# Kernel tuning notes

Hardware: AMD Instinct MI355X
Metric: run time of the kernel (lower is better)

The kernel has to match this reference:

```python
import jax, jax.numpy as jnp
import numpy as np

Q, B, S, D, H, DFF = 300, 2, 4096, 256, 8, 2048
HD = D // H
SMOOTH = 8.0


def _ln(x, g, b):
    m = x.mean(-1, keepdims=True)
    v = ((x - m) ** 2).mean(-1, keepdims=True)
    return (x - m) / jnp.sqrt(v + 1e-5) * g + b


def _mha(q, k, v, Wi, bi, Wo, bo, bias=None):
    # q: [L,B,D], k/v: [S,B,D]; torch nn.MultiheadAttention math (eval mode)
    L, Bb, Dd = q.shape
    Sl = k.shape[0]
    Wq, Wk, Wv = jnp.split(Wi, 3, axis=0)
    bq, bk, bv = jnp.split(bi, 3)
    qp = ((q @ Wq.T + bq) * (HD ** -0.5)).reshape(L, Bb * H, HD).transpose(1, 0, 2)
    kp = (k @ Wk.T + bk).reshape(Sl, Bb * H, HD).transpose(1, 0, 2)
    vp = (v @ Wv.T + bv).reshape(Sl, Bb * H, HD).transpose(1, 0, 2)
    logits = jnp.einsum('bld,bsd->bls', qp, kp)  # [B*H, L, S]
    if bias is not None:
        logits = logits + bias  # Gaussian distance bias added pre-softmax
    attn = jax.nn.softmax(logits, axis=-1)
    out = jnp.einsum('bls,bsd->bld', attn, vp).transpose(1, 0, 2).reshape(L, Bb, Dd)
    return out @ Wo.T + bo


def setup_inputs():
    key = jax.random.key(0)
    ks = iter(jax.random.split(key, 48))
    def nrm(shape, s=1.0):
        return jax.random.normal(next(ks), shape, dtype=jnp.float32) * s
    inp = {}
    inp['grid'] = jax.random.uniform(next(ks), (S, 1, 2), dtype=jnp.float32) * 32.0
    inp['h_w'] = jax.random.uniform(next(ks), (B, 2), dtype=jnp.float32) * 800.0
    inp['tgt'] = nrm((Q, B, D))
    inp['memory'] = nrm((S, B, D))
    inp['pos'] = nrm((S, B, D))
    inp['query_pos'] = nrm((Q, B, D))
    inp['reshape_outputs1'] = jax.random.randint(next(ks), (Q, 4), 0, 3, dtype=jnp.int32)
    inp['reshape_outputs2'] = jax.random.randint(next(ks), (Q, 4), 0, 3, dtype=jnp.int32)
    w = 0.02
    inp['sa_Wi'] = nrm((3 * D, D), w); inp['sa_bi'] = jnp.zeros((3 * D,), jnp.float32)
    inp['sa_Wo'] = nrm((D, D), w); inp['sa_bo'] = jnp.zeros((D,), jnp.float32)
    inp['ca_Wi'] = nrm((3 * D, D), w); inp['ca_bi'] = jnp.zeros((3 * D,), jnp.float32)
    inp['ca_Wo'] = nrm((D, D), w); inp['ca_bo'] = jnp.zeros((D,), jnp.float32)
    inp['W1'] = nrm((DFF, D), w); inp['b1'] = jnp.zeros((DFF,), jnp.float32)
    inp['W2'] = nrm((D, DFF), w); inp['b2'] = jnp.zeros((D,), jnp.float32)
    for n in ['n1', 'n2', 'n3', 'n4']:
        inp[n + 'g'] = jnp.ones((D,), jnp.float32)
        inp[n + 'b'] = jnp.zeros((D,), jnp.float32)
    inp['p1_W0'] = nrm((256, 256), w); inp['p1_b0'] = jnp.zeros((256,), jnp.float32)
    inp['p1_W1'] = nrm((256, 256), w); inp['p1_b1'] = jnp.zeros((256,), jnp.float32)
    inp['p1_W2'] = nrm((2, 256), w); inp['p1_b2'] = jnp.zeros((2,), jnp.float32)
    inp['p2W'] = nrm((16, D), w); inp['p2b'] = jnp.zeros((16,), jnp.float32)
    inp['p3W'] = nrm((16, D), w); inp['p3b'] = jnp.zeros((16,), jnp.float32)
    return inp


def reference(grid, h_w, tgt, memory, pos, query_pos, reshape_outputs1, reshape_outputs2,
              sa_Wi, sa_bi, sa_Wo, sa_bo, ca_Wi, ca_bi, ca_Wo, ca_bo,
              W1, b1, W2, b2, n1g, n1b, n2g, n2b, n3g, n3b, n4g, n4b,
              p1_W0, p1_b0, p1_W1, p1_b1, p1_W2, p1_b2, p2W, p2b, p3W, p3b):
    out = _ln(tgt + query_pos, n4g, n4b)                          # [Q,B,D]
    point_offset = out @ p2W.T + p2b                              # [Q,B,16]
    qk = tgt + query_pos
    tgt2 = _mha(qk, qk, tgt, sa_Wi, sa_bi, sa_Wo, sa_bo)
    x = _ln(tgt + tgt2, n1g, n1b)
    # point1 MLP (layer_index == 0)
    h1 = jax.nn.relu(out @ p1_W0.T + p1_b0)
    h2 = jax.nn.relu(h1 @ p1_W1.T + p1_b1)
    ref_inter = h2 @ p1_W2.T + p1_b2                              # [Q,B,2]
    ref = h_w * jax.nn.sigmoid(ref_inter) / 32.0                  # [Q,B,2]
    ref = jnp.tile(ref, (1, 1, 8))                                # [Q,B,16]
    point = (ref + point_offset).reshape(Q, B * 8, 2)             # [Q,B*8,2]
    dist = (point[:, None, :, :] - grid[None]) ** 2               # [Q,S,B*8,2]
    scale = out @ p3W.T + p3b                                     # type3: [Q,B,16]
    scale = (scale * scale).reshape(Q, B * 8, 2)[:, None]         # [Q,1,B*8,2]
    dist = (dist * scale).sum(-1)                                 # [Q,S,B*8]
    gaussian = -jnp.abs(dist) / SMOOTH
    gbias = jnp.transpose(gaussian, (2, 0, 1))                    # [B*8,Q,S]
    # masked object query from reshape_outputs
    oq = jnp.transpose(query_pos, (1, 0, 2))                      # [B,Q,D]
    m1 = jnp.any(reshape_outputs1 == 0, axis=1)                   # [Q]
    m2 = jnp.any(reshape_outputs2 == 0, axis=1)
    oq1 = jnp.where(m1[:, None], 0.0, oq[0])
    oq2 = jnp.where(m2[:, None], 0.0, oq[1])
    new_oq = jnp.stack([oq1, oq2], axis=1)                        # [Q,2,D]
    tgt2 = _mha(x + query_pos, memory + pos, memory, ca_Wi, ca_bi, ca_Wo, ca_bo, bias=gbias)
    tgt3 = _mha(x + new_oq, memory + pos, memory, ca_Wi, ca_bi, ca_Wo, ca_bo, bias=gbias)
    x = _ln(x + tgt2, n2g, n2b)
    ff = jax.nn.relu(x @ W1.T + b1) @ W2.T + b2
    x = _ln(x + ff, n3g, n3b)
    return (x, ref_inter, ref, tgt3)
```

## Files before the change

### kernel.cpp

```cpp
#include <hip/hip_runtime.h>
#include <hip/hip_bf16.h>
#include <math.h>

#define QN 300
#define BN 2
#define SN 4096
#define DN 256
#define HN 8
#define HD 32
#define BH 16
#define DFF 2048

__device__ inline float wred_max(float v) {
#pragma unroll
    for (int m = 32; m > 0; m >>= 1) v = fmaxf(v, __shfl_xor(v, m));
    return v;
}
__device__ inline float wred_sum(float v) {
#pragma unroll
    for (int m = 32; m > 0; m >>= 1) v += __shfl_xor(v, m);
    return v;
}

__global__ __launch_bounds__(256) void addln_kernel(
    const float* __restrict__ a, const float* __restrict__ b,
    const float* __restrict__ g, const float* __restrict__ be,
    float* __restrict__ out_ln, float* __restrict__ out_sum)
{
    int row = blockIdx.x;
    int t = threadIdx.x;
    float v = a[row * DN + t] + b[row * DN + t];
    if (out_sum) out_sum[row * DN + t] = v;
    float s = wred_sum(v);
    float s2 = wred_sum(v * v);
    __shared__ float ws1[4], ws2[4];
    int wave = t >> 6, lane = t & 63;
    if (lane == 0) { ws1[wave] = s; ws2[wave] = s2; }
    __syncthreads();
    float S1 = ws1[0] + ws1[1] + ws1[2] + ws1[3];
    float S2 = ws2[0] + ws2[1] + ws2[2] + ws2[3];
    float mean = S1 * (1.0f / DN);
    float var = S2 * (1.0f / DN) - mean * mean;
    float inv = rsqrtf(var + 1e-5f);
    out_ln[row * DN + t] = (v - mean) * inv * g[t] + be[t];
}

__global__ void addvec_kernel(const float* __restrict__ a, const float* __restrict__ b,
                              float* __restrict__ c, int n4)
{
    int i = blockIdx.x * blockDim.x + threadIdx.x;
    int stride = gridDim.x * blockDim.x;
    for (; i < n4; i += stride) {
        float4 x = ((const float4*)a)[i];
        float4 y = ((const float4*)b)[i];
        float4 z; z.x = x.x + y.x; z.y = x.y + y.y; z.z = x.z + y.z; z.w = x.w + y.w;
        ((float4*)c)[i] = z;
    }
}

__global__ __launch_bounds__(256) void build_xq_xo(
    const float* __restrict__ x1, const float* __restrict__ qp,
    const int* __restrict__ ro1, const int* __restrict__ ro2,
    float* __restrict__ xq, float* __restrict__ xo)
{
    int row = blockIdx.x, t = threadIdx.x;
    int q = row >> 1, b = row & 1;
    const int* ro = b ? ro2 : ro1;
    bool msk = (ro[q * 4 + 0] == 0) || (ro[q * 4 + 1] == 0) ||
               (ro[q * 4 + 2] == 0) || (ro[q * 4 + 3] == 0);
    float xv = x1[row * DN + t], qv = qp[row * DN + t];
    xq[row * DN + t] = xv + qv;
    xo[row * DN + t] = xv + (msk ? 0.0f : qv);
}

template <int MODE>
__global__ __launch_bounds__(256) void gemm_nt(
    const float* __restrict__ A, const float* __restrict__ W,
    const float* __restrict__ bias, float* __restrict__ C,
    int M, int N, int K, int seqLen, float scale)
{
    __shared__ float As[16][68];
    __shared__ float Bs[16][68];
    int bm = blockIdx.x * 64;
    int bn = blockIdx.y * 64;
    int t = threadIdx.x;
    int lr = t >> 2;
    int lc = (t & 3) << 2;
    int tm = (t >> 4) << 2;
    int tn = (t & 15) << 2;
    float acc[4][4] = {};
    for (int k0 = 0; k0 < K; k0 += 16) {
        int arow = bm + lr;
        float4 av = make_float4(0, 0, 0, 0);
        if (arow < M) av = *(const float4*)&A[(size_t)arow * K + k0 + lc];
        float4 bv = *(const float4*)&W[(size_t)(bn + lr) * K + k0 + lc];
        __syncthreads();
        As[lc + 0][lr] = av.x; As[lc + 1][lr] = av.y; As[lc + 2][lr] = av.z; As[lc + 3][lr] = av.w;
        Bs[lc + 0][lr] = bv.x; Bs[lc + 1][lr] = bv.y; Bs[lc + 2][lr] = bv.z; Bs[lc + 3][lr] = bv.w;
        __syncthreads();
#pragma unroll
        for (int kk = 0; kk < 16; kk++) {
            float4 a = *(const float4*)&As[kk][tm];
            float4 b = *(const float4*)&Bs[kk][tn];
            acc[0][0] = fmaf(a.x, b.x, acc[0][0]); acc[0][1] = fmaf(a.x, b.y, acc[0][1]);
            acc[0][2] = fmaf(a.x, b.z, acc[0][2]); acc[0][3] = fmaf(a.x, b.w, acc[0][3]);
            acc[1][0] = fmaf(a.y, b.x, acc[1][0]); acc[1][1] = fmaf(a.y, b.y, acc[1][1]);
            acc[1][2] = fmaf(a.y, b.z, acc[1][2]); acc[1][3] = fmaf(a.y, b.w, acc[1][3]);
            acc[2][0] = fmaf(a.z, b.x, acc[2][0]); acc[2][1] = fmaf(a.z, b.y, acc[2][1]);
            acc[2][2] = fmaf(a.z, b.z, acc[2][2]); acc[2][3] = fmaf(a.z, b.w, acc[2][3]);
            acc[3][0] = fmaf(a.w, b.x, acc[3][0]); acc[3][1] = fmaf(a.w, b.y, acc[3][1]);
            acc[3][2] = fmaf(a.w, b.z, acc[3][2]); acc[3][3] = fmaf(a.w, b.w, acc[3][3]);
        }
    }
#pragma unroll
    for (int i = 0; i < 4; i++) {
        int m = bm + tm + i;
        if (m >= M) continue;
#pragma unroll
        for (int j = 0; j < 4; j++) {
            int n = bn + tn + j;
            float v = acc[i][j] + bias[n];
            if (MODE == 1) v = fmaxf(v, 0.0f);
            if (MODE == 2) {
                v *= scale;
                int b = m & 1, seq = m >> 1, h = n >> 5, hd = n & 31;
                C[((size_t)(b * 8 + h) * seqLen + seq) * 32 + hd] = v;
            } else {
                C[(size_t)m * N + n] = v;
            }
        }
    }
}

template <int MODE>
__global__ __launch_bounds__(256) void gemm_small(
    const float* __restrict__ A, const float* __restrict__ W,
    const float* __restrict__ bias, float* __restrict__ C,
    int M, int N, int K, int seqLen, float scale)
{
    __shared__ float As[16][36];
    __shared__ float Bs[16][36];
    int bm = blockIdx.x * 32;
    int bn = blockIdx.y * 32;
    int t = threadIdx.x;
    int sr = (t & 127) >> 2;
    int sc = (t & 3) << 2;
    bool isB = t >= 128;
    int tm = (t >> 4) << 1;
    int tn = (t & 15) << 1;
    float acc[2][2] = {};
    int srcRow = (isB ? bn : bm) + sr;
    int lim = isB ? N : M;
    const float* src = isB ? W : A;
    for (int k0 = 0; k0 < K; k0 += 16) {
        float4 v = make_float4(0, 0, 0, 0);
        if (srcRow < lim) v = *(const float4*)&src[(size_t)srcRow * K + k0 + sc];
        __syncthreads();
        float (*Ts)[36] = isB ? Bs : As;
        Ts[sc + 0][sr] = v.x; Ts[sc + 1][sr] = v.y; Ts[sc + 2][sr] = v.z; Ts[sc + 3][sr] = v.w;
        __syncthreads();
#pragma unroll
        for (int kk = 0; kk < 16; kk++) {
            float2 a = *(const float2*)&As[kk][tm];
            float2 b = *(const float2*)&Bs[kk][tn];
            acc[0][0] = fmaf(a.x, b.x, acc[0][0]); acc[0][1] = fmaf(a.x, b.y, acc[0][1]);
            acc[1][0] = fmaf(a.y, b.x, acc[1][0]); acc[1][1] = fmaf(a.y, b.y, acc[1][1]);
        }
    }
#pragma unroll
    for (int i = 0; i < 2; i++) {
        int m = bm + tm + i;
        if (m >= M) continue;
#pragma unroll
        for (int j = 0; j < 2; j++) {
            int n = bn + tn + j;
            float v = acc[i][j] + bias[n];
            if (MODE == 1) v = fmaxf(v, 0.0f);
            if (MODE == 2) {
                v *= scale;
                int b = m & 1, seq = m >> 1, h = n >> 5, hd = n & 31;
                C[((size_t)(b * 8 + h) * seqLen + seq) * 32 + hd] = v;
            } else {
                C[(size_t)m * N + n] = v;
            }
        }
    }
}

__global__ __launch_bounds__(64) void small_heads(
    const float* __restrict__ ln4, const float* __restrict__ h2,
    const float* __restrict__ p2W, const float* __restrict__ p2b,
    const float* __restrict__ p3W, const float* __restrict__ p3b,
    const float* __restrict__ p1W2, const float* __restrict__ p1b2,
    const float* __restrict__ h_w,
    float* __restrict__ ref_inter_out, float* __restrict__ ref_out,
    float* __restrict__ point, float* __restrict__ scale2)
{
    int row = blockIdx.x;
    int lane = threadIdx.x;
    __shared__ float rA[DN], rH[DN];
    __shared__ float po[16], sc[16], ri[2];
#pragma unroll
    for (int i = 0; i < 4; i++) {
        rA[lane + i * 64] = ln4[row * DN + lane + i * 64];
        rH[lane + i * 64] = h2[row * DN + lane + i * 64];
    }
    __syncthreads();
    for (int j = 0; j < 16; j++) {
        float p = 0;
#pragma unroll
        for (int i = 0; i < 4; i++) { int d = lane + i * 64; p = fmaf(rA[d], p2W[j * DN + d], p); }
        p = wred_sum(p);
        if (lane == 0) po[j] = p + p2b[j];
    }
    for (int j = 0; j < 16; j++) {
        float p = 0;
#pragma unroll
        for (int i = 0; i < 4; i++) { int d = lane + i * 64; p = fmaf(rA[d], p3W[j * DN + d], p); }
        p = wred_sum(p);
        if (lane == 0) sc[j] = p + p3b[j];
    }
    for (int j = 0; j < 2; j++) {
        float p = 0;
#pragma unroll
        for (int i = 0; i < 4; i++) { int d = lane + i * 64; p = fmaf(rH[d], p1W2[j * DN + d], p); }
        p = wred_sum(p);
        if (lane == 0) ri[j] = p + p1b2[j];
    }
    __syncthreads();
    int q = row >> 1, b = row & 1;
    float sig0 = 1.0f / (1.0f + expf(-ri[0]));
    float sig1 = 1.0f / (1.0f + expf(-ri[1]));
    float rx = h_w[b * 2 + 0] * sig0 * (1.0f / 32.0f);
    float ry = h_w[b * 2 + 1] * sig1 * (1.0f / 32.0f);
    if (lane < 2) ref_inter_out[row * 2 + lane] = ri[lane];
    if (lane < 16) {
        float rc = (lane & 1) ? ry : rx;
        ref_out[row * 16 + lane] = rc;
        int pidx = (q * 16 + b * 8 + (lane >> 1)) * 2 + (lane & 1);
        point[pidx] = rc + po[lane];
        float s = sc[lane];
        scale2[pidx] = s * s;
    }
}

template <bool BIAS>
__global__ __launch_bounds__(256) void attn_split(
    const float* __restrict__ qp, const float* __restrict__ kp, const float* __restrict__ vp,
    const float* __restrict__ point, const float* __restrict__ scale2,
    const float* __restrict__ grid_xy,
    float* __restrict__ pacc, float* __restrict__ pm, float* __restrict__ pl,
    int S, int L, int tilesPerChunk, int ROWS)
{
    const int bh = blockIdx.y;
    const int q0 = blockIdx.x * 16;
    const int chunk = blockIdx.z;
    const int nT = (S + 63) >> 6;
    const int t_begin = chunk * tilesPerChunk;
    const int t_end = min(nT, t_begin + tilesPerChunk);

    __shared__ float Qs[16][36];
    __shared__ float Ks[64][36];
    __shared__ float Vsf[64 * 32];
    __shared__ float Ps[16][68];
    __shared__ float sf_s[16];
    __shared__ float pt_s[16][2], sc_s[16][2];

    int t = threadIdx.x;
    int wave = t >> 6, lane = t & 63;

    {
        int qi = t >> 4, d = (t & 15) * 2;
        int gq = q0 + qi;
        float2 v = make_float2(0, 0);
        if (gq < L) v = *(const float2*)&qp[((size_t)bh * L + gq) * 32 + d];
        Qs[qi][d] = v.x; Qs[qi][d + 1] = v.y;
        if (BIAS && t < 32) {
            int qi2 = t >> 1, c = t & 1;
            int gq2 = q0 + qi2;
            pt_s[qi2][c] = (gq2 < L) ? point[(gq2 * 16 + bh) * 2 + c] : 0.0f;
            sc_s[qi2][c] = (gq2 < L) ? scale2[(gq2 * 16 + bh) * 2 + c] : 0.0f;
        }
    }
    float m_run[4], l_run[4];
#pragma unroll
    for (int r = 0; r < 4; r++) { m_run[r] = -INFINITY; l_run[r] = 0.0f; }
    int pq = t >> 4, pd = t & 15;
    float2 acc = make_float2(0.0f, 0.0f);
    __syncthreads();

    for (int tt = t_begin; tt < t_end; tt++) {
        int s0 = tt << 6;
#pragma unroll
        for (int rep = 0; rep < 2; rep++) {
            int f = t + rep * 256;
            int s = f >> 3, dc = (f & 7) * 4;
            int gs = s0 + s;
            float4 kv = make_float4(0, 0, 0, 0), vv = make_float4(0, 0, 0, 0);
            if (gs < S) {
                kv = *(const float4*)&kp[((size_t)bh * S + gs) * 32 + dc];
                vv = *(const float4*)&vp[((size_t)bh * S + gs) * 32 + dc];
            }
            Ks[s][dc + 0] = kv.x; Ks[s][dc + 1] = kv.y; Ks[s][dc + 2] = kv.z; Ks[s][dc + 3] = kv.w;
            Vsf[s * 32 + dc + 0] = vv.x; Vsf[s * 32 + dc + 1] = vv.y;
            Vsf[s * 32 + dc + 2] = vv.z; Vsf[s * 32 + dc + 3] = vv.w;
        }
        float gx = 0, gy = 0;
        if (BIAS) {
            int gs = s0 + lane;
            if (gs < S) { gx = grid_xy[gs * 2 + 0]; gy = grid_xy[gs * 2 + 1]; }
        }
        __syncthreads();

        float kreg[32];
#pragma unroll
        for (int d4 = 0; d4 < 8; d4++) {
            float4 kk = *(const float4*)&Ks[lane][d4 * 4];
            kreg[d4 * 4 + 0] = kk.x; kreg[d4 * 4 + 1] = kk.y;
            kreg[d4 * 4 + 2] = kk.z; kreg[d4 * 4 + 3] = kk.w;
        }
        bool svalid = (s0 + lane) < S;
#pragma unroll
        for (int r = 0; r < 4; r++) {
            int qi = wave * 4 + r;
            float sum = 0;
#pragma unroll
            for (int d4 = 0; d4 < 8; d4++) {
                float4 qv = *(const float4*)&Qs[qi][d4 * 4];
                sum = fmaf(qv.x, kreg[d4 * 4 + 0], sum);
                sum = fmaf(qv.y, kreg[d4 * 4 + 1], sum);
                sum = fmaf(qv.z, kreg[d4 * 4 + 2], sum);
                sum = fmaf(qv.w, kreg[d4 * 4 + 3], sum);
            }
            if (BIAS) {
                float dx = pt_s[qi][0] - gx, dy = pt_s[qi][1] - gy;
                sum -= (sc_s[qi][0] * dx * dx + sc_s[qi][1] * dy * dy) * 0.125f;
            }
            float l = svalid ? sum : -INFINITY;
            float tmax = wred_max(l);
            float m_new = fmaxf(m_run[r], tmax);
            float p = expf(l - m_new);
            float psum = wred_sum(p);
            float sfv = expf(m_run[r] - m_new);
            l_run[r] = l_run[r] * sfv + psum;
            m_run[r] = m_new;
            Ps[qi][lane] = p;
            if (lane == 0) sf_s[qi] = sfv;
        }
        __syncthreads();

        {
            float sfv = sf_s[pq];
            acc.x *= sfv; acc.y *= sfv;
#pragma unroll
            for (int s4 = 0; s4 < 16; s4++) {
                float4 p4 = *(const float4*)&Ps[pq][s4 * 4];
                float2 v0 = *(const float2*)&Vsf[(s4 * 4 + 0) * 32 + pd * 2];
                float2 v1 = *(const float2*)&Vsf[(s4 * 4 + 1) * 32 + pd * 2];
                float2 v2 = *(const float2*)&Vsf[(s4 * 4 + 2) * 32 + pd * 2];
                float2 v3 = *(const float2*)&Vsf[(s4 * 4 + 3) * 32 + pd * 2];
                acc.x = fmaf(p4.x, v0.x, acc.x); acc.y = fmaf(p4.x, v0.y, acc.y);
                acc.x = fmaf(p4.y, v1.x, acc.x); acc.y = fmaf(p4.y, v1.y, acc.y);
                acc.x = fmaf(p4.z, v2.x, acc.x); acc.y = fmaf(p4.z, v2.y, acc.y);
                acc.x = fmaf(p4.w, v3.x, acc.x); acc.y = fmaf(p4.w, v3.y, acc.y);
            }
        }
        __syncthreads();
    }

    if (lane == 0) {
#pragma unroll
        for (int r = 0; r < 4; r++) {
            int row = q0 + wave * 4 + r;
            int pidx = (chunk * 16 + bh) * ROWS + row;
            pm[pidx] = m_run[r];
            pl[pidx] = l_run[r];
        }
    }
    {
        int row = q0 + pq;
        int pidx = (chunk * 16 + bh) * ROWS + row;
        *(float2*)&pacc[(size_t)pidx * 32 + pd * 2] = acc;
    }
}

__global__ __launch_bounds__(256) void attn_combine(
    const float* __restrict__ pacc, const float* __restrict__ pm, const float* __restrict__ pl,
    float* __restrict__ outbuf, int NS, int ROWS, int L)
{
    int gid = blockIdx.x * 256 + threadIdx.x;
    if (gid >= 16 * L * 32) return;
    int d = gid & 31;
    int pr = gid >> 5;
    int bh = pr / L;
    int row = pr - bh * L;
    float M = -INFINITY;
    for (int c = 0; c < NS; c++) M = fmaxf(M, pm[(c * 16 + bh) * ROWS + row]);
    float Lt = 0.0f, a = 0.0f;
    for (int c = 0; c < NS; c++) {
        int pidx = (c * 16 + bh) * ROWS + row;
        float w = expf(pm[pidx] - M);
        Lt = fmaf(pl[pidx], w, Lt);
        a = fmaf(pacc[(size_t)pidx * 32 + d], w, a);
    }
    int b = bh >> 3, h = bh & 7;
    outbuf[((size_t)row * BN + b) * DN + h * 32 + d] = a / Lt;
}

#define OFF_QK      0
#define OFF_LN4     153600
#define OFF_H1      307200
#define OFF_TMP     307200
#define OFF_H2      460800
#define OFF_POINT   614400
#define OFF_SCALE2  624000
#define OFF_SAQ     633600
#define OFF_SAK     787200
#define OFF_SAV     940800
#define OFF_AOUT    1094400
#define OFF_X1      1248000
#define OFF_MP      1401600
#define OFF_PACC    1401600
#define OFF_PM      2646784
#define OFF_PL      2685696
#define OFF_CAK     3498752
#define OFF_CAV     5595904
#define OFF_XQ      7693056
#define OFF_XO      7846656
#define OFF_AOUT2   8000256
#define OFF_AOUT3   8153856
#define OFF_X2      8307456
#define OFF_FFH     8461056

extern "C" void kernel_launch(void* const* d_in, const int* in_sizes, int n_in,
                              void* d_out, int out_size, void* d_ws, size_t ws_size,
                              hipStream_t stream)
{
    const float* grid_in   = (const float*)d_in[0];
    const float* h_w       = (const float*)d_in[1];
    const float* tgt       = (const float*)d_in[2];
    const float* memory    = (const float*)d_in[3];
    const float* pos       = (const float*)d_in[4];
    const float* query_pos = (const float*)d_in[5];
    const int*   ro1       = (const int*)d_in[6];
    const int*   ro2       = (const int*)d_in[7];
    const float* sa_Wi = (const float*)d_in[8];
    const float* sa_bi = (const float*)d_in[9];
    const float* sa_Wo = (const float*)d_in[10];
    const float* sa_bo = (const float*)d_in[11];
    const float* ca_Wi = (const float*)d_in[12];
    const float* ca_bi = (const float*)d_in[13];
    const float* ca_Wo = (const float*)d_in[14];
    const float* ca_bo = (const float*)d_in[15];
    const float* W1 = (const float*)d_in[16];
    const float* b1 = (const float*)d_in[17];
    const float* W2 = (const float*)d_in[18];
    const float* b2 = (const float*)d_in[19];
    const float* n1g = (const float*)d_in[20];
    const float* n1b = (const float*)d_in[21];
    const float* n2g = (const float*)d_in[22];
    const float* n2b = (const float*)d_in[23];
    const float* n3g = (const float*)d_in[24];
    const float* n3b = (const float*)d_in[25];
    const float* n4g = (const float*)d_in[26];
    const float* n4b = (const float*)d_in[27];
    const float* p1_W0 = (const float*)d_in[28];
    const float* p1_b0 = (const float*)d_in[29];
    const float* p1_W1 = (const float*)d_in[30];
    const float* p1_b1 = (const float*)d_in[31];
    const float* p1_W2 = (const float*)d_in[32];
    const float* p1_b2 = (const float*)d_in[33];
    const float* p2W = (const float*)d_in[34];
    const float* p2b = (const float*)d_in[35];
    const float* p3W = (const float*)d_in[36];
    const float* p3b = (const float*)d_in[37];

    float* ws  = (float*)d_ws;
    float* out = (float*)d_out;
    const float qscale = 0.1767766952966369f;

    dim3 g600(600), b256(256);
    dim3 gS(19, 8);
    dim3 gFF1(19, 64);
    dim3 gKV(128, 4);

    addln_kernel<<<g600, b256, 0, stream>>>(tgt, query_pos, n4g, n4b, ws + OFF_LN4, ws + OFF_QK);
    gemm_small<1><<<gS, b256, 0, stream>>>(ws + OFF_LN4, p1_W0, p1_b0, ws + OFF_H1, 600, 256, 256, 0, 1.f);
    gemm_small<1><<<gS, b256, 0, stream>>>(ws + OFF_H1, p1_W1, p1_b1, ws + OFF_H2, 600, 256, 256, 0, 1.f);
    small_heads<<<g600, dim3(64), 0, stream>>>(ws + OFF_LN4, ws + OFF_H2, p2W, p2b, p3W, p3b,
                                               p1_W2, p1_b2, h_w,
                                               out + 153600, out + 154800,
                                               ws + OFF_POINT, ws + OFF_SCALE2);
    gemm_small<2><<<gS, b256, 0, stream>>>(ws + OFF_QK, sa_Wi,          sa_bi,       ws + OFF_SAQ, 600, 256, 256, 300, qscale);
    gemm_small<2><<<gS, b256, 0, stream>>>(ws + OFF_QK, sa_Wi + 65536,  sa_bi + 256, ws + OFF_SAK, 600, 256, 256, 300, 1.f);
    gemm_small<2><<<gS, b256, 0, stream>>>(tgt,         sa_Wi + 131072, sa_bi + 512, ws + OFF_SAV, 600, 256, 256, 300, 1.f);
    attn_split<false><<<dim3(19, 16, 2), b256, 0, stream>>>(
        ws + OFF_SAQ, ws + OFF_SAK, ws + OFF_SAV, nullptr, nullptr, nullptr,
        ws + OFF_PACC, ws + OFF_PM, ws + OFF_PL, 300, 300, 3, 304);
    attn_combine<<<g600, b256, 0, stream>>>(ws + OFF_PACC, ws + OFF_PM, ws + OFF_PL,
                                            ws + OFF_AOUT, 2, 304, 300);
    gemm_small<0><<<gS, b256, 0, stream>>>(ws + OFF_AOUT, sa_Wo, sa_bo, ws + OFF_TMP, 600, 256, 256, 0, 1.f);
    addln_kernel<<<g600, b256, 0, stream>>>(tgt, ws + OFF_TMP, n1g, n1b, ws + OFF_X1, nullptr);
    addvec_kernel<<<dim3(2048), b256, 0, stream>>>(memory, pos, ws + OFF_MP, (SN * BN * DN) / 4);
    gemm_nt<2><<<gKV, b256, 0, stream>>>(ws + OFF_MP, ca_Wi + 65536,  ca_bi + 256, ws + OFF_CAK, 8192, 256, 256, 4096, 1.f);
    gemm_nt<2><<<gKV, b256, 0, stream>>>(memory,      ca_Wi + 131072, ca_bi + 512, ws + OFF_CAV, 8192, 256, 256, 4096, 1.f);
    build_xq_xo<<<g600, b256, 0, stream>>>(ws + OFF_X1, query_pos, ro1, ro2, ws + OFF_XQ, ws + OFF_XO);
    gemm_small<2><<<gS, b256, 0, stream>>>(ws + OFF_XQ, ca_Wi, ca_bi, ws + OFF_SAQ, 600, 256, 256, 300, qscale);
    gemm_small<2><<<gS, b256, 0, stream>>>(ws + OFF_XO, ca_Wi, ca_bi, ws + OFF_SAK, 600, 256, 256, 300, qscale);
    attn_split<true><<<dim3(19, 16, 8), b256, 0, stream>>>(
        ws + OFF_SAQ, ws + OFF_CAK, ws + OFF_CAV,
        ws + OFF_POINT, ws + OFF_SCALE2, grid_in,
        ws + OFF_PACC, ws + OFF_PM, ws + OFF_PL, 4096, 300, 8, 304);
    attn_combine<<<g600, b256, 0, stream>>>(ws + OFF_PACC, ws + OFF_PM, ws + OFF_PL,
                                            ws + OFF_AOUT2, 8, 304, 300);
    attn_split<true><<<dim3(19, 16, 8), b256, 0, stream>>>(
        ws + OFF_SAK, ws + OFF_CAK, ws + OFF_CAV,
        ws + OFF_POINT, ws + OFF_SCALE2, grid_in,
        ws + OFF_PACC, ws + OFF_PM, ws + OFF_PL, 4096, 300, 8, 304);
    attn_combine<<<g600, b256, 0, stream>>>(ws + OFF_PACC, ws + OFF_PM, ws + OFF_PL,
                                            ws + OFF_AOUT3, 8, 304, 300);
    gemm_small<0><<<gS, b256, 0, stream>>>(ws + OFF_AOUT2, ca_Wo, ca_bo, ws + OFF_TMP, 600, 256, 256, 0, 1.f);
    gemm_small<0><<<gS, b256, 0, stream>>>(ws + OFF_AOUT3, ca_Wo, ca_bo, out + 164400, 600, 256, 256, 0, 1.f);
    addln_kernel<<<g600, b256, 0, stream>>>(ws + OFF_X1, ws + OFF_TMP, n2g, n2b, ws + OFF_X2, nullptr);
    gemm_small<1><<<gFF1, b256, 0, stream>>>(ws + OFF_X2, W1, b1, ws + OFF_FFH, 600, 2048, 256, 0, 1.f);
    gemm_small<0><<<gS, b256, 0, stream>>>(ws + OFF_FFH, W2, b2, ws + OFF_TMP, 600, 256, 2048, 0, 1.f);
    addln_kernel<<<g600, b256, 0, stream>>>(ws + OFF_X2, ws + OFF_TMP, n3g, n3b, out, nullptr);
}
```

Measured before the change: 711.7 us.

## Use bf16 MFMA for cross-attention K/V projections and one attention pass

Converts memory, memory+pos and the K/V weights to bf16 and computes the cross-attention K/V projections with a 16x16x32 bf16 MFMA GEMM that writes bf16 head-major outputs. The first cross-attention pass reads the bf16 K/V and widens it into shared memory, using a transposed V layout. The second pass is replaced by a new kernel that computes QK^T with MFMA over 64-query tiles, adds the Gaussian bias and runs online softmax. This is meant to cut the FP32 FMA work and the K/V memory traffic, at the cost of bf16 precision in K, V and one set of queries, plus extra conversion kernels.

```diff
diff --git a/kernel.cpp b/kernel.cpp
--- a/kernel.cpp
+++ b/kernel.cpp
@@ -11,15 +11,23 @@
 #define BH 16
 #define DFF 2048
 
-__device__ inline float wred_max(float v) {
-#pragma unroll
-    for (int m = 32; m > 0; m >>= 1) v = fmaxf(v, __shfl_xor(v, m));
-    return v;
-}
+typedef __attribute__((ext_vector_type(8))) short s16x8;
+typedef __attribute__((ext_vector_type(4))) float f32x4;
+
 __device__ inline float wred_sum(float v) {
 #pragma unroll
     for (int m = 32; m > 0; m >>= 1) v += __shfl_xor(v, m);
     return v;
+}
+__device__ inline ushort f2b(float x) {
+    union { __hip_bfloat16 h; ushort u; } c;
+    c.h = __float2bfloat16(x);
+    return c.u;
+}
+__device__ inline float b2f(ushort u) {
+    union { unsigned int i; float f; } c;
+    c.i = ((unsigned int)u) << 16;
+    return c.f;
 }
 
 __global__ __launch_bounds__(256) void addln_kernel(
@@ -45,16 +53,29 @@
     out_ln[row * DN + t] = (v - mean) * inv * g[t] + be[t];
 }
 
-__global__ void addvec_kernel(const float* __restrict__ a, const float* __restrict__ b,
-                              float* __restrict__ c, int n4)
+__global__ void f2bf_kernel(const float* __restrict__ in, ushort* __restrict__ out, int n4)
+{
+    int i = blockIdx.x * blockDim.x + threadIdx.x;
+    int stride = gridDim.x * blockDim.x;
+    for (; i < n4; i += stride) {
+        float4 x = ((const float4*)in)[i];
+        ushort4 o;
+        o.x = f2b(x.x); o.y = f2b(x.y); o.z = f2b(x.z); o.w = f2b(x.w);
+        ((ushort4*)out)[i] = o;
+    }
+}
+__global__ void addvec_bf16_kernel(const float* __restrict__ a, const float* __restrict__ b,
+                                   ushort* __restrict__ out, int n4)
 {
     int i = blockIdx.x * blockDim.x + threadIdx.x;
     int stride = gridDim.x * blockDim.x;
     for (; i < n4; i += stride) {
         float4 x = ((const float4*)a)[i];
         float4 y = ((const float4*)b)[i];
-        float4 z; z.x = x.x + y.x; z.y = x.y + y.y; z.z = x.z + y.z; z.w = x.w + y.w;
-        ((float4*)c)[i] = z;
+        ushort4 o;
+        o.x = f2b(x.x + y.x); o.y = f2b(x.y + y.y);
+        o.z = f2b(x.z + y.z); o.w = f2b(x.w + y.w);
+        ((ushort4*)out)[i] = o;
     }
 }
 
@@ -71,65 +92,6 @@
     float xv = x1[row * DN + t], qv = qp[row * DN + t];
     xq[row * DN + t] = xv + qv;
     xo[row * DN + t] = xv + (msk ? 0.0f : qv);
-}
-
-template <int MODE>
-__global__ __launch_bounds__(256) void gemm_nt(
-    const float* __restrict__ A, const float* __restrict__ W,
-    const float* __restrict__ bias, float* __restrict__ C,
-    int M, int N, int K, int seqLen, float scale)
-{
-    __shared__ float As[16][68];
-    __shared__ float Bs[16][68];
-    int bm = blockIdx.x * 64;
-    int bn = blockIdx.y * 64;
-    int t = threadIdx.x;
-    int lr = t >> 2;
-    int lc = (t & 3) << 2;
-    int tm = (t >> 4) << 2;
-    int tn = (t & 15) << 2;
-    float acc[4][4] = {};
-    for (int k0 = 0; k0 < K; k0 += 16) {
-        int arow = bm + lr;
-        float4 av = make_float4(0, 0, 0, 0);
-        if (arow < M) av = *(const float4*)&A[(size_t)arow * K + k0 + lc];
-        float4 bv = *(const float4*)&W[(size_t)(bn + lr) * K + k0 + lc];
-        __syncthreads();
-        As[lc + 0][lr] = av.x; As[lc + 1][lr] = av.y; As[lc + 2][lr] = av.z; As[lc + 3][lr] = av.w;
-        Bs[lc + 0][lr] = bv.x; Bs[lc + 1][lr] = bv.y; Bs[lc + 2][lr] = bv.z; Bs[lc + 3][lr] = bv.w;
-        __syncthreads();
-#pragma unroll
-        for (int kk = 0; kk < 16; kk++) {
-            float4 a = *(const float4*)&As[kk][tm];
-            float4 b = *(const float4*)&Bs[kk][tn];
-            acc[0][0] = fmaf(a.x, b.x, acc[0][0]); acc[0][1] = fmaf(a.x, b.y, acc[0][1]);
-            acc[0][2] = fmaf(a.x, b.z, acc[0][2]); acc[0][3] = fmaf(a.x, b.w, acc[0][3]);
-            acc[1][0] = fmaf(a.y, b.x, acc[1][0]); acc[1][1] = fmaf(a.y, b.y, acc[1][1]);
-            acc[1][2] = fmaf(a.y, b.z, acc[1][2]); acc[1][3] = fmaf(a.y, b.w, acc[1][3]);
-            acc[2][0] = fmaf(a.z, b.x, acc[2][0]); acc[2][1] = fmaf(a.z, b.y, acc[2][1]);
-            acc[2][2] = fmaf(a.z, b.z, acc[2][2]); acc[2][3] = fmaf(a.z, b.w, acc[2][3]);
-            acc[3][0] = fmaf(a.w, b.x, acc[3][0]); acc[3][1] = fmaf(a.w, b.y, acc[3][1]);
-            acc[3][2] = fmaf(a.w, b.z, acc[3][2]); acc[3][3] = fmaf(a.w, b.w, acc[3][3]);
-        }
-    }
-#pragma unroll
-    for (int i = 0; i < 4; i++) {
-        int m = bm + tm + i;
-        if (m >= M) continue;
-#pragma unroll
-        for (int j = 0; j < 4; j++) {
-            int n = bn + tn + j;
-            float v = acc[i][j] + bias[n];
-            if (MODE == 1) v = fmaxf(v, 0.0f);
-            if (MODE == 2) {
-                v *= scale;
-                int b = m & 1, seq = m >> 1, h = n >> 5, hd = n & 31;
-                C[((size_t)(b * 8 + h) * seqLen + seq) * 32 + hd] = v;
-            } else {
-                C[(size_t)m * N + n] = v;
-            }
-        }
-    }
 }
 
 template <int MODE>
@@ -180,9 +142,58 @@
                 v *= scale;
                 int b = m & 1, seq = m >> 1, h = n >> 5, hd = n & 31;
                 C[((size_t)(b * 8 + h) * seqLen + seq) * 32 + hd] = v;
+            } else if (MODE == 4) {
+                v *= scale;
+                int b = m & 1, seq = m >> 1, h = n >> 5, hd = n & 31;
+                ushort* Cb = (ushort*)C;
+                Cb[((size_t)(b * 8 + h) * seqLen + seq) * 32 + hd] = f2b(v);
             } else {
                 C[(size_t)m * N + n] = v;
             }
+        }
+    }
+}
+
+__global__ __launch_bounds__(256) void gemm_bf16_mfma(
+    const ushort* __restrict__ A, const ushort* __restrict__ W,
+    const float* __restrict__ bias, ushort* __restrict__ C, int seqLen)
+{
+    __shared__ ushort As[64][40];
+    __shared__ ushort Ws[64][40];
+    int bm = blockIdx.x * 64;
+    int bn = blockIdx.y * 64;
+    int t = threadIdx.x;
+    int w = t >> 6, lane = t & 63;
+    int lr = lane & 15, lg = lane >> 4;
+    int sr = t >> 2, sg = t & 3;
+
+    f32x4 acc[4];
+#pragma unroll
+    for (int f = 0; f < 4; f++) acc[f] = (f32x4)0.0f;
+
+    for (int k0 = 0; k0 < 256; k0 += 32) {
+        int4 av = *(const int4*)&A[((size_t)(bm + sr)) * 256 + k0 + sg * 8];
+        int4 wv = *(const int4*)&W[((size_t)(bn + sr)) * 256 + k0 + sg * 8];
+        __syncthreads();
+        *(int4*)&As[sr][sg * 8] = av;
+        *(int4*)&Ws[sr][sg * 8] = wv;
+        __syncthreads();
+        s16x8 af = *(const s16x8*)&As[w * 16 + lr][lg * 8];
+#pragma unroll
+        for (int f = 0; f < 4; f++) {
+            s16x8 bf = *(const s16x8*)&Ws[f * 16 + lr][lg * 8];
+            acc[f] = __builtin_amdgcn_mfma_f32_16x16x32_bf16(af, bf, acc[f], 0, 0, 0);
+        }
+    }
+#pragma unroll
+    for (int f = 0; f < 4; f++) {
+#pragma unroll
+        for (int j = 0; j < 4; j++) {
+            int m = bm + w * 16 + lg * 4 + j;
+            int n = bn + f * 16 + lr;
+            float v = acc[f][j] + bias[n];
+            int b = m & 1, seq = m >> 1, h = n >> 5, hd = n & 31;
+            C[(((size_t)(b * 8 + h) * seqLen) + seq) * 32 + hd] = f2b(v);
         }
     }
 }
@@ -244,9 +255,9 @@
     }
 }
 
-template <bool BIAS>
+template <bool BIAS, bool BF16KV>
 __global__ __launch_bounds__(256) void attn_split(
-    const float* __restrict__ qp, const float* __restrict__ kp, const float* __restrict__ vp,
+    const float* __restrict__ qp, const void* __restrict__ kp_, const void* __restrict__ vp_,
     const float* __restrict__ point, const float* __restrict__ scale2,
     const float* __restrict__ grid_xy,
     float* __restrict__ pacc, float* __restrict__ pm, float* __restrict__ pl,
@@ -261,7 +272,7 @@
 
     __shared__ float Qs[16][36];
     __shared__ float Ks[64][36];
-    __shared__ float Vsf[64 * 32];
+    __shared__ float Vt[32][68];
     __shared__ float Ps[16][68];
     __shared__ float sf_s[16];
     __shared__ float pt_s[16][2], sc_s[16][2];
@@ -291,19 +302,39 @@
 
     for (int tt = t_begin; tt < t_end; tt++) {
         int s0 = tt << 6;
-#pragma unroll
-        for (int rep = 0; rep < 2; rep++) {
-            int f = t + rep * 256;
-            int s = f >> 3, dc = (f & 7) * 4;
+        if (BF16KV) {
+            const ushort* kp = (const ushort*)kp_;
+            const ushort* vp = (const ushort*)vp_;
+            int s = t >> 2, dg = (t & 3) * 8;
             int gs = s0 + s;
-            float4 kv = make_float4(0, 0, 0, 0), vv = make_float4(0, 0, 0, 0);
+            int4 kv = make_int4(0, 0, 0, 0), vv = make_int4(0, 0, 0, 0);
             if (gs < S) {
-                kv = *(const float4*)&kp[((size_t)bh * S + gs) * 32 + dc];
-                vv = *(const float4*)&vp[((size_t)bh * S + gs) * 32 + dc];
-            }
-            Ks[s][dc + 0] = kv.x; Ks[s][dc + 1] = kv.y; Ks[s][dc + 2] = kv.z; Ks[s][dc + 3] = kv.w;
-            Vsf[s * 32 + dc + 0] = vv.x; Vsf[s * 32 + dc + 1] = vv.y;
-            Vsf[s * 32 + dc + 2] = vv.z; Vsf[s * 32 + dc + 3] = vv.w;
+                kv = *(const int4*)&kp[((size_t)bh * S + gs) * 32 + dg];
+                vv = *(const int4*)&vp[((size_t)bh * S + gs) * 32 + dg];
+            }
+            union { int4 v; ushort u[8]; } ck, cv;
+            ck.v = kv; cv.v = vv;
+#pragma unroll
+            for (int jj = 0; jj < 8; jj++) {
+                Ks[s][dg + jj] = b2f(ck.u[jj]);
+                Vt[dg + jj][s] = b2f(cv.u[jj]);
+            }
+        } else {
+            const float* kp = (const float*)kp_;
+            const float* vp = (const float*)vp_;
+#pragma unroll
+            for (int rep = 0; rep < 2; rep++) {
+                int f = t + rep * 256;
+                int s = f >> 3, dc = (f & 7) * 4;
+                int gs = s0 + s;
+                float4 kv = make_float4(0, 0, 0, 0), vv = make_float4(0, 0, 0, 0);
+                if (gs < S) {
+                    kv = *(const float4*)&kp[((size_t)bh * S + gs) * 32 + dc];
+                    vv = *(const float4*)&vp[((size_t)bh * S + gs) * 32 + dc];
+                }
+                Ks[s][dc + 0] = kv.x; Ks[s][dc + 1] = kv.y; Ks[s][dc + 2] = kv.z; Ks[s][dc + 3] = kv.w;
+                Vt[dc + 0][s] = vv.x; Vt[dc + 1][s] = vv.y; Vt[dc + 2][s] = vv.z; Vt[dc + 3][s] = vv.w;
+            }
         }
         float gx = 0, gy = 0;
         if (BIAS) {
@@ -337,11 +368,13 @@
                 sum -= (sc_s[qi][0] * dx * dx + sc_s[qi][1] * dy * dy) * 0.125f;
             }
             float l = svalid ? sum : -INFINITY;
-            float tmax = wred_max(l);
+            float tmax = l;
+#pragma unroll
+            for (int m = 32; m > 0; m >>= 1) tmax = fmaxf(tmax, __shfl_xor(tmax, m));
             float m_new = fmaxf(m_run[r], tmax);
-            float p = expf(l - m_new);
+            float p = __expf(l - m_new);
             float psum = wred_sum(p);
-            float sfv = expf(m_run[r] - m_new);
+            float sfv = __expf(m_run[r] - m_new);
             l_run[r] = l_run[r] * sfv + psum;
             m_run[r] = m_new;
             Ps[qi][lane] = p;
@@ -351,19 +384,19 @@
 
         {
             float sfv = sf_s[pq];
-            acc.x *= sfv; acc.y *= sfv;
+            float ax = acc.x * sfv, ay = acc.y * sfv;
+            int d0 = pd * 2;
 #pragma unroll
             for (int s4 = 0; s4 < 16; s4++) {
                 float4 p4 = *(const float4*)&Ps[pq][s4 * 4];
-                float2 v0 = *(const float2*)&Vsf[(s4 * 4 + 0) * 32 + pd * 2];
-                float2 v1 = *(const float2*)&Vsf[(s4 * 4 + 1) * 32 + pd * 2];
-                float2 v2 = *(const float2*)&Vsf[(s4 * 4 + 2) * 32 + pd * 2];
-                float2 v3 = *(const float2*)&Vsf[(s4 * 4 + 3) * 32 + pd * 2];
-                acc.x = fmaf(p4.x, v0.x, acc.x); acc.y = fmaf(p4.x, v0.y, acc.y);
-                acc.x = fmaf(p4.y, v1.x, acc.x); acc.y = fmaf(p4.y, v1.y, acc.y);
-                acc.x = fmaf(p4.z, v2.x, acc.x); acc.y = fmaf(p4.z, v2.y, acc.y);
-                acc.x = fmaf(p4.w, v3.x, acc.x); acc.y = fmaf(p4.w, v3.y, acc.y);
-            }
+                float4 va = *(const float4*)&Vt[d0][s4 * 4];
+                float4 vb = *(const float4*)&Vt[d0 + 1][s4 * 4];
+                ax = fmaf(p4.x, va.x, ax); ax = fmaf(p4.y, va.y, ax);
+                ax = fmaf(p4.z, va.z, ax); ax = fmaf(p4.w, va.w, ax);
+                ay = fmaf(p4.x, vb.x, ay); ay = fmaf(p4.y, vb.y, ay);
+                ay = fmaf(p4.z, vb.z, ay); ay = fmaf(p4.w, vb.w, ay);
+            }
+            acc.x = ax; acc.y = ay;
         }
         __syncthreads();
     }
@@ -372,15 +405,206 @@
 #pragma unroll
         for (int r = 0; r < 4; r++) {
             int row = q0 + wave * 4 + r;
-            int pidx = (chunk * 16 + bh) * ROWS + row;
+            size_t pidx = (size_t)(chunk * 16 + bh) * ROWS + row;
             pm[pidx] = m_run[r];
             pl[pidx] = l_run[r];
         }
     }
     {
         int row = q0 + pq;
-        int pidx = (chunk * 16 + bh) * ROWS + row;
-        *(float2*)&pacc[(size_t)pidx * 32 + pd * 2] = acc;
+        size_t pidx = (size_t)(chunk * 16 + bh) * ROWS + row;
+        *(float2*)&pacc[pidx * 32 + pd * 2] = acc;
+    }
+}
+
+template <bool BIAS>
+__global__ __launch_bounds__(256) void attn_qkmfma(
+    const ushort* __restrict__ qp, const ushort* __restrict__ kp, const ushort* __restrict__ vp,
+    const float* __restrict__ point, const float* __restrict__ scale2,
+    const float* __restrict__ grid_xy,
+    float* __restrict__ pacc, float* __restrict__ pm, float* __restrict__ pl,
+    int S, int L, int tilesPerChunk, int ROWS)
+{
+    const int bh = blockIdx.y;
+    const int q0 = blockIdx.x * 64;
+    const int chunk = blockIdx.z;
+    const int nT = (S + 63) >> 6;
+    const int t_begin = chunk * tilesPerChunk;
+    const int t_end = min(nT, t_begin + tilesPerChunk);
+
+    __shared__ ushort Ks[64][40];
+    __shared__ float Vt[32][68];
+    __shared__ float Ps[64][68];
+    __shared__ float sf_s[64];
+    __shared__ float gq2[64][2];
+    __shared__ float qc[64][4];
+
+    int t = threadIdx.x;
+    int w = t >> 6, lane = t & 63;
+    int lr = lane & 15, lg = lane >> 4;
+    int sr = t >> 2, sg = t & 3;
+
+    s16x8 qfrag;
+    {
+        int qrow = q0 + w * 16 + lr;
+        if (qrow < L) qfrag = *(const s16x8*)&qp[((size_t)bh * L + qrow) * 32 + lg * 8];
+        else qfrag = (s16x8)(short)0;
+    }
+
+    float px[4], py[4], sx[4], sy[4];
+    if (BIAS) {
+        if (t < 64) {
+            int q = q0 + t;
+            float a = 0, b = 0, c = 0, d = 0;
+            if (q < L) {
+                a = point[(q * 16 + bh) * 2 + 0];
+                b = point[(q * 16 + bh) * 2 + 1];
+                c = scale2[(q * 16 + bh) * 2 + 0];
+                d = scale2[(q * 16 + bh) * 2 + 1];
+            }
+            qc[t][0] = a; qc[t][1] = b; qc[t][2] = c; qc[t][3] = d;
+        }
+        __syncthreads();
+#pragma unroll
+        for (int j = 0; j < 4; j++) {
+            int ql = w * 16 + lg * 4 + j;
+            px[j] = qc[ql][0]; py[j] = qc[ql][1];
+            sx[j] = qc[ql][2]; sy[j] = qc[ql][3];
+        }
+    }
+
+    float m_run[4], l_run[4];
+#pragma unroll
+    for (int j = 0; j < 4; j++) { m_run[j] = -INFINITY; l_run[j] = 0.0f; }
+
+    int q2 = (t >> 3) * 2;
+    int dq = (t & 7) * 4;
+    float accv0[4] = {0, 0, 0, 0};
+    float accv1[4] = {0, 0, 0, 0};
+
+    for (int tt = t_begin; tt < t_end; tt++) {
+        int s0 = tt << 6;
+        int gs = s0 + sr;
+        int4 kv = make_int4(0, 0, 0, 0), vv = make_int4(0, 0, 0, 0);
+        if (gs < S) {
+            kv = *(const int4*)&kp[((size_t)bh * S + gs) * 32 + sg * 8];
+            vv = *(const int4*)&vp[((size_t)bh * S + gs) * 32 + sg * 8];
+        }
+        __syncthreads();
+        *(int4*)&Ks[sr][sg * 8] = kv;
+        {
+            union { int4 v; ushort u[8]; } cv; cv.v = vv;
+            int d0 = sg * 8;
+#pragma unroll
+            for (int jj = 0; jj < 8; jj++) Vt[d0 + jj][sr] = b2f(cv.u[jj]);
+        }
+        if (BIAS && t < 64) {
+            gq2[t][0] = grid_xy[(size_t)(s0 + t) * 2 + 0];
+            gq2[t][1] = grid_xy[(size_t)(s0 + t) * 2 + 1];
+        }
+        __syncthreads();
+
+        f32x4 sfrag[4];
+#pragma unroll
+        for (int f = 0; f < 4; f++) {
+            s16x8 kf = *(const s16x8*)&Ks[f * 16 + lr][lg * 8];
+            sfrag[f] = __builtin_amdgcn_mfma_f32_16x16x32_bf16(qfrag, kf, (f32x4)0.0f, 0, 0, 0);
+        }
+#pragma unroll
+        for (int f = 0; f < 4; f++) {
+            int gsc = s0 + f * 16 + lr;
+            if (BIAS) {
+                float gx = gq2[f * 16 + lr][0];
+                float gy = gq2[f * 16 + lr][1];
+#pragma unroll
+                for (int j = 0; j < 4; j++) {
+                    float dx = px[j] - gx, dy = py[j] - gy;
+                    sfrag[f][j] -= (sx[j] * dx * dx + sy[j] * dy * dy) * 0.125f;
+                }
+            }
+            if (gsc >= S) {
+#pragma unroll
+                for (int j = 0; j < 4; j++) sfrag[f][j] = -INFINITY;
+            }
+        }
+        float sfv[4];
+#pragma unroll
+        for (int j = 0; j < 4; j++) {
+            float mx = fmaxf(fmaxf(sfrag[0][j], sfrag[1][j]), fmaxf(sfrag[2][j], sfrag[3][j]));
+            mx = fmaxf(mx, __shfl_xor(mx, 1));
+            mx = fmaxf(mx, __shfl_xor(mx, 2));
+            mx = fmaxf(mx, __shfl_xor(mx, 4));
+            mx = fmaxf(mx, __shfl_xor(mx, 8));
+            float mnew = fmaxf(m_run[j], mx);
+            sfv[j] = __expf(m_run[j] - mnew);
+            m_run[j] = mnew;
+            float ps = 0.0f;
+#pragma unroll
+            for (int f = 0; f < 4; f++) {
+                float p = __expf(sfrag[f][j] - mnew);
+                sfrag[f][j] = p;
+                ps += p;
+            }
+            ps += __shfl_xor(ps, 1);
+            ps += __shfl_xor(ps, 2);
+            ps += __shfl_xor(ps, 4);
+            ps += __shfl_xor(ps, 8);
+            l_run[j] = l_run[j] * sfv[j] + ps;
+        }
+#pragma unroll
+        for (int f = 0; f < 4; f++) {
+#pragma unroll
+            for (int j = 0; j < 4; j++) {
+                Ps[w * 16 + lg * 4 + j][f * 16 + lr] = sfrag[f][j];
+            }
+        }
+        if (lr == 0) {
+#pragma unroll
+            for (int j = 0; j < 4; j++) sf_s[w * 16 + lg * 4 + j] = sfv[j];
+        }
+        __syncthreads();
+
+        {
+            float sf0 = sf_s[q2], sf1 = sf_s[q2 + 1];
+#pragma unroll
+            for (int d = 0; d < 4; d++) { accv0[d] *= sf0; accv1[d] *= sf1; }
+#pragma unroll
+            for (int s4 = 0; s4 < 16; s4++) {
+                float4 p0 = *(const float4*)&Ps[q2][s4 * 4];
+                float4 p1 = *(const float4*)&Ps[q2 + 1][s4 * 4];
+#pragma unroll
+                for (int d = 0; d < 4; d++) {
+                    float4 v4 = *(const float4*)&Vt[dq + d][s4 * 4];
+                    accv0[d] = fmaf(p0.x, v4.x, accv0[d]);
+                    accv0[d] = fmaf(p0.y, v4.y, accv0[d]);
+                    accv0[d] = fmaf(p0.z, v4.z, accv0[d]);
+                    accv0[d] = fmaf(p0.w, v4.w, accv0[d]);
+                    accv1[d] = fmaf(p1.x, v4.x, accv1[d]);
+                    accv1[d] = fmaf(p1.y, v4.y, accv1[d]);
+                    accv1[d] = fmaf(p1.z, v4.z, accv1[d]);
+                    accv1[d] = fmaf(p1.w, v4.w, accv1[d]);
+                }
+            }
+        }
+    }
+
+    if (lr == 0) {
+#pragma unroll
+        for (int j = 0; j < 4; j++) {
+            int row = q0 + w * 16 + lg * 4 + j;
+            size_t pidx = (size_t)(chunk * 16 + bh) * ROWS + row;
+            pm[pidx] = m_run[j];
+            pl[pidx] = l_run[j];
+        }
+    }
+    {
+        size_t pidx0 = (size_t)(chunk * 16 + bh) * ROWS + (q0 + q2);
+        size_t pidx1 = pidx0 + 1;
+#pragma unroll
+        for (int d = 0; d < 4; d++) {
+            pacc[pidx0 * 32 + dq + d] = accv0[d];
+            pacc[pidx1 * 32 + dq + d] = accv1[d];
+        }
     }
 }
 
@@ -395,13 +619,13 @@
     int bh = pr / L;
     int row = pr - bh * L;
     float M = -INFINITY;
-    for (int c = 0; c < NS; c++) M = fmaxf(M, pm[(c * 16 + bh) * ROWS + row]);
+    for (int c = 0; c < NS; c++) M = fmaxf(M, pm[(size_t)(c * 16 + bh) * ROWS + row]);
     float Lt = 0.0f, a = 0.0f;
     for (int c = 0; c < NS; c++) {
-        int pidx = (c * 16 + bh) * ROWS + row;
-        float w = expf(pm[pidx] - M);
-        Lt = fmaf(pl[pidx], w, Lt);
-        a = fmaf(pacc[(size_t)pidx * 32 + d], w, a);
+        size_t pidx = (size_t)(c * 16 + bh) * ROWS + row;
+        float wgt = __expf(pm[pidx] - M);
+        Lt = fmaf(pl[pidx], wgt, Lt);
+        a = fmaf(pacc[pidx * 32 + d], wgt, a);
     }
     int b = bh >> 3, h = bh & 7;
     outbuf[((size_t)row * BN + b) * DN + h * 32 + d] = a / Lt;
@@ -409,28 +633,32 @@
 
 #define OFF_QK      0
 #define OFF_LN4     153600
-#define OFF_H1      307200
 #define OFF_TMP     307200
-#define OFF_H2      460800
-#define OFF_POINT   614400
-#define OFF_SCALE2  624000
-#define OFF_SAQ     633600
-#define OFF_SAK     787200
-#define OFF_SAV     940800
-#define OFF_AOUT    1094400
-#define OFF_X1      1248000
-#define OFF_MP      1401600
-#define OFF_PACC    1401600
-#define OFF_PM      2646784
-#define OFF_PL      2685696
-#define OFF_CAK     3498752
-#define OFF_CAV     5595904
-#define OFF_XQ      7693056
-#define OFF_XO      7846656
-#define OFF_AOUT2   8000256
-#define OFF_AOUT3   8153856
-#define OFF_X2      8307456
-#define OFF_FFH     8461056
+#define OFF_H1      460800
+#define OFF_H2      614400
+#define OFF_POINT   768000
+#define OFF_SCALE2  777600
+#define OFF_SAQ     787200
+#define OFF_SAK     940800
+#define OFF_SAV     1094400
+#define OFF_AOUT    1248000
+#define OFF_X1      1401600
+#define OFF_PACC    1555200
+#define OFF_PM      2865920
+#define OFF_PL      2906880
+#define OFF_MEMB    2947840
+#define OFF_MPB     3996416
+#define OFF_WKVB    5044992
+#define OFF_CAKB    5110528
+#define OFF_CAVB    6159104
+#define OFF_XQ      7207680
+#define OFF_XO      7361280
+#define OFF_CAQ     7514880
+#define OFF_CAQ2B   7668480
+#define OFF_AOUT2   7745280
+#define OFF_AOUT3   7898880
+#define OFF_X2      8052480
+#define OFF_FFH     8206080
 
 extern "C" void kernel_launch(void* const* d_in, const int* in_sizes, int n_in,
                               void* d_out, int out_size, void* d_ws, size_t ws_size,
@@ -479,6 +707,13 @@
     float* out = (float*)d_out;
     const float qscale = 0.1767766952966369f;
 
+    ushort* memb  = (ushort*)(ws + OFF_MEMB);
+    ushort* mpb   = (ushort*)(ws + OFF_MPB);
+    ushort* wkvb  = (ushort*)(ws + OFF_WKVB);
+    ushort* cakb  = (ushort*)(ws + OFF_CAKB);
+    ushort* cavb  = (ushort*)(ws + OFF_CAVB);
+    ushort* caq2b = (ushort*)(ws + OFF_CAQ2B);
+
     dim3 g600(600), b256(256);
     dim3 gS(19, 8);
     dim3 gFF1(19, 64);
@@ -494,31 +729,31 @@
     gemm_small<2><<<gS, b256, 0, stream>>>(ws + OFF_QK, sa_Wi,          sa_bi,       ws + OFF_SAQ, 600, 256, 256, 300, qscale);
     gemm_small<2><<<gS, b256, 0, stream>>>(ws + OFF_QK, sa_Wi + 65536,  sa_bi + 256, ws + OFF_SAK, 600, 256, 256, 300, 1.f);
     gemm_small<2><<<gS, b256, 0, stream>>>(tgt,         sa_Wi + 131072, sa_bi + 512, ws + OFF_SAV, 600, 256, 256, 300, 1.f);
-    attn_split<false><<<dim3(19, 16, 2), b256, 0, stream>>>(
+    attn_split<false, false><<<dim3(19, 16, 2), b256, 0, stream>>>(
         ws + OFF_SAQ, ws + OFF_SAK, ws + OFF_SAV, nullptr, nullptr, nullptr,
         ws + OFF_PACC, ws + OFF_PM, ws + OFF_PL, 300, 300, 3, 304);
     attn_combine<<<g600, b256, 0, stream>>>(ws + OFF_PACC, ws + OFF_PM, ws + OFF_PL,
                                             ws + OFF_AOUT, 2, 304, 300);
     gemm_small<0><<<gS, b256, 0, stream>>>(ws + OFF_AOUT, sa_Wo, sa_bo, ws + OFF_TMP, 600, 256, 256, 0, 1.f);
     addln_kernel<<<g600, b256, 0, stream>>>(tgt, ws + OFF_TMP, n1g, n1b, ws + OFF_X1, nullptr);
-    addvec_kernel<<<dim3(2048), b256, 0, stream>>>(memory, pos, ws + OFF_MP, (SN * BN * DN) / 4);
-    gemm_nt<2><<<gKV, b256, 0, stream>>>(ws + OFF_MP, ca_Wi + 65536,  ca_bi + 256, ws + OFF_CAK, 8192, 256, 256, 4096, 1.f);
-    gemm_nt<2><<<gKV, b256, 0, stream>>>(memory,      ca_Wi + 131072, ca_bi + 512, ws + OFF_CAV, 8192, 256, 256, 4096, 1.f);
+    f2bf_kernel<<<dim3(1024), b256, 0, stream>>>(memory, memb, (SN * BN * DN) / 4);
+    addvec_bf16_kernel<<<dim3(1024), b256, 0, stream>>>(memory, pos, mpb, (SN * BN * DN) / 4);
+    f2bf_kernel<<<dim3(128), b256, 0, stream>>>(ca_Wi + 65536, wkvb, (2 * DN * DN) / 4);
+    gemm_bf16_mfma<<<gKV, b256, 0, stream>>>(mpb, wkvb, ca_bi + 256, cakb, 4096);
+    gemm_bf16_mfma<<<gKV, b256, 0, stream>>>(memb, wkvb + 65536, ca_bi + 512, cavb, 4096);
     build_xq_xo<<<g600, b256, 0, stream>>>(ws + OFF_X1, query_pos, ro1, ro2, ws + OFF_XQ, ws + OFF_XO);
-    gemm_small<2><<<gS, b256, 0, stream>>>(ws + OFF_XQ, ca_Wi, ca_bi, ws + OFF_SAQ, 600, 256, 256, 300, qscale);
-    gemm_small<2><<<gS, b256, 0, stream>>>(ws + OFF_XO, ca_Wi, ca_bi, ws + OFF_SAK, 600, 256, 256, 300, qscale);
-    attn_split<true><<<dim3(19, 16, 8), b256, 0, stream>>>(
-        ws + OFF_SAQ, ws + OFF_CAK, ws + OFF_CAV,
-        ws + OFF_POINT, ws + OFF_SCALE2, grid_in,
+    gemm_small<2><<<gS, b256, 0, stream>>>(ws + OFF_XQ, ca_Wi, ca_bi, ws + OFF_CAQ, 600, 256, 256, 300, qscale);
+    gemm_small<4><<<gS, b256, 0, stream>>>(ws + OFF_XO, ca_Wi, ca_bi, (float*)caq2b, 600, 256, 256, 300, qscale);
+    attn_split<true, true><<<dim3(19, 16, 8), b256, 0, stream>>>(
+        ws + OFF_CAQ, cakb, cavb, ws + OFF_POINT, ws + OFF_SCALE2, grid_in,
         ws + OFF_PACC, ws + OFF_PM, ws + OFF_PL, 4096, 300, 8, 304);
     attn_combine<<<g600, b256, 0, stream>>>(ws + OFF_PACC, ws + OFF_PM, ws + OFF_PL,
                                             ws + OFF_AOUT2, 8, 304, 300);
-    attn_split<true><<<dim3(19, 16, 8), b256, 0, stream>>>(
-        ws + OFF_SAK, ws + OFF_CAK, ws + OFF_CAV,
-        ws + OFF_POINT, ws + OFF_SCALE2, grid_in,
-        ws + OFF_PACC, ws + OFF_PM, ws + OFF_PL, 4096, 300, 8, 304);
+    attn_qkmfma<true><<<dim3(5, 16, 8), b256, 0, stream>>>(
+        caq2b, cakb, cavb, ws + OFF_POINT, ws + OFF_SCALE2, grid_in,
+        ws + OFF_PACC, ws + OFF_PM, ws + OFF_PL, 4096, 300, 8, 320);
     attn_combine<<<g600, b256, 0, stream>>>(ws + OFF_PACC, ws + OFF_PM, ws + OFF_PL,
-                                            ws + OFF_AOUT3, 8, 304, 300);
+                                            ws + OFF_AOUT3, 8, 320, 300);
     gemm_small<0><<<gS, b256, 0, stream>>>(ws + OFF_AOUT2, ca_Wo, ca_bo, ws + OFF_TMP, 600, 256, 256, 0, 1.f);
     gemm_small<0><<<gS, b256, 0, stream>>>(ws + OFF_AOUT3, ca_Wo, ca_bo, out + 164400, 600, 256, 256, 0, 1.f);
     addln_kernel<<<g600, b256, 0, stream>>>(ws + OFF_X1, ws + OFF_TMP, n2g, n2b, ws + OFF_X2, nullptr);
```

Result: slower. 730.8 us (+2.7%).
